# Kernel optimization log

Hardware: AMD Instinct MI355X
Metric: run time of the kernel (lower is better)

The kernel has to match this reference:

```python
import jax, jax.numpy as jnp
import numpy as np

NEG = -1000000000.0


def setup_inputs() -> dict:
    key = jax.random.key(0)
    k1, k2, k3, k4, k5 = jax.random.split(key, 5)
    B, T, D, Q = 8, 2048, 1024, 128
    x = jax.random.normal(k1, (B, T, D), dtype=jnp.float32)
    attn_mask = jax.random.randint(k2, (B, T), 0, 2).astype(jnp.bool_)
    s = 1.0 / np.sqrt(D)
    Wq = jax.random.normal(k3, (Q, D), dtype=jnp.float32) * s
    Wk = jax.random.normal(k4, (Q, D), dtype=jnp.float32) * s
    Wv = jax.random.normal(k5, (Q, D), dtype=jnp.float32) * s
    return {"x": x, "attn_mask": attn_mask, "Wq": Wq, "Wk": Wk, "Wv": Wv}


def reference(x, attn_mask, Wq, Wk, Wv):
    # x: (B,T,D); W*: (Q,D) torch Linear weights (y = x @ W.T)
    q = jnp.einsum('btd,qd->btq', x, Wq)
    k = jnp.einsum('btd,qd->btq', x, Wk)
    v = jnp.einsum('btd,qd->btq', x, Wv)
    logits = jnp.einsum('btq,bsq->bts', q, k)  # (B,T,T), no 1/sqrt(d) scaling (matches source)
    m = attn_mask[:, None, :]  # (B,1,T) broadcasts over query dim, == repeat(1,T,1)
    logits = jnp.where(m, logits, NEG)
    A = jax.nn.softmax(logits, axis=-1)
    A = jnp.where(m, A, 0.0)
    return jnp.einsum('bts,bsq->btq', A, v)
```

## Files before the change

### kernel.cpp

```cpp
#include <hip/hip_runtime.h>
#include <hip/hip_bf16.h>
#include <hip/hip_fp16.h>

typedef _Float16 half8 __attribute__((ext_vector_type(8)));
typedef _Float16 half4v __attribute__((ext_vector_type(4)));
typedef float float4v __attribute__((ext_vector_type(4)));

#define MFMA_F16(a, b, c) __builtin_amdgcn_mfma_f32_16x16x32_f16((a), (b), (c), 0, 0, 0)

#define GLDS16(gp, lp) \
    __builtin_amdgcn_global_load_lds((const __attribute__((address_space(1))) unsigned int*)(gp), \
                                     (__attribute__((address_space(3))) unsigned int*)(lp), 16, 0, 0)

#define BATCH 8
#define SEQ   2048
#define DIM   1024
#define QD    128
#define BT    (BATCH * SEQ)
#define NSPLIT 4
#define KSPAN (SEQ / NSPLIT)

__device__ __forceinline__ float dpp_max16(float x) {
    int v;
    v = __builtin_amdgcn_update_dpp(0, __float_as_int(x), 0xB1, 0xF, 0xF, false);
    x = fmaxf(x, __int_as_float(v));
    v = __builtin_amdgcn_update_dpp(0, __float_as_int(x), 0x4E, 0xF, 0xF, false);
    x = fmaxf(x, __int_as_float(v));
    v = __builtin_amdgcn_update_dpp(0, __float_as_int(x), 0x141, 0xF, 0xF, false);
    x = fmaxf(x, __int_as_float(v));
    v = __builtin_amdgcn_update_dpp(0, __float_as_int(x), 0x140, 0xF, 0xF, false);
    x = fmaxf(x, __int_as_float(v));
    return x;
}

__global__ __launch_bounds__(256) void cvt_w_kernel(const float* __restrict__ Wq,
                                                    const float* __restrict__ Wk,
                                                    const float* __restrict__ Wv,
                                                    _Float16* __restrict__ Wh) {
    const float* src = (blockIdx.y == 0) ? Wq : ((blockIdx.y == 1) ? Wk : Wv);
    int i = blockIdx.x * 256 + threadIdx.x;
    float4 f = ((const float4*)src)[i];
    half4v h = {(_Float16)f.x, (_Float16)f.y, (_Float16)f.z, (_Float16)f.w};
    ((half4v*)(Wh + (size_t)blockIdx.y * QD * DIM))[i] = h;
}

__global__ __launch_bounds__(256, 3) void proj_kernel(
    const float* __restrict__ x,
    const _Float16* __restrict__ Wh,
    _Float16* __restrict__ q_out,
    _Float16* __restrict__ k_out,
    _Float16* __restrict__ vt_out)
{
    __shared__ _Float16 As[64 * 64];
    __shared__ _Float16 Bs[128 * 64];

    const int tid  = threadIdx.x;
    const int lane = tid & 63;
    const int wave = tid >> 6;
    const int quad = lane >> 4;
    const int l15  = lane & 15;
    const int wr   = wave >> 1;
    const int wc   = wave & 1;

    const int which = blockIdx.y;
    const _Float16* W = Wh + (size_t)which * QD * DIM;
    const int row0 = blockIdx.x * 64;

    const int ar  = tid >> 2;
    const int ac4 = tid & 3;
    const float4* xp = (const float4*)(x + (size_t)(row0 + ar) * DIM) + ac4 * 4;
    const int ga = ac4 * 2;
    const int sw = ar & 7;
    _Float16* aw0 = &As[ar * 64 + ((ga     ^ sw) * 8)];
    _Float16* aw1 = &As[ar * 64 + (((ga|1) ^ sw) * 8)];

    float4v acc[2][4];
#pragma unroll
    for (int rf = 0; rf < 2; rf++)
#pragma unroll
        for (int n = 0; n < 4; n++)
            acc[rf][n] = (float4v){0.f, 0.f, 0.f, 0.f};

    for (int kk = 0; kk < DIM; kk += 64) {
        int kb = kk >> 2;
        float4 a0 = xp[kb + 0];
        float4 a1 = xp[kb + 1];
        float4 a2 = xp[kb + 2];
        float4 a3 = xp[kb + 3];
        __syncthreads();
#pragma unroll
        for (int c = 0; c < 4; c++) {
            int ci = wave * 256 + c * 64 + lane;
            int r  = ci >> 3;
            int g  = (ci & 7) ^ (r & 7);
            GLDS16(W + (size_t)r * DIM + kk + g * 8, &Bs[(wave * 256 + c * 64) * 8]);
        }
        half8 h0, h1;
        h0[0] = (_Float16)a0.x; h0[1] = (_Float16)a0.y; h0[2] = (_Float16)a0.z; h0[3] = (_Float16)a0.w;
        h0[4] = (_Float16)a1.x; h0[5] = (_Float16)a1.y; h0[6] = (_Float16)a1.z; h0[7] = (_Float16)a1.w;
        h1[0] = (_Float16)a2.x; h1[1] = (_Float16)a2.y; h1[2] = (_Float16)a2.z; h1[3] = (_Float16)a2.w;
        h1[4] = (_Float16)a3.x; h1[5] = (_Float16)a3.y; h1[6] = (_Float16)a3.z; h1[7] = (_Float16)a3.w;
        *(half8*)aw0 = h0;
        *(half8*)aw1 = h1;
        __syncthreads();

        half8 af[2][2], bf[4][2];
#pragma unroll
        for (int rf = 0; rf < 2; rf++)
#pragma unroll
            for (int kc = 0; kc < 2; kc++) {
                int r = wr * 32 + rf * 16 + l15;
                int g = (kc * 4 + quad) ^ (r & 7);
                af[rf][kc] = *(const half8*)&As[r * 64 + g * 8];
            }
#pragma unroll
        for (int n = 0; n < 4; n++)
#pragma unroll
            for (int kc = 0; kc < 2; kc++) {
                int r = wc * 64 + n * 16 + l15;
                int g = (kc * 4 + quad) ^ (r & 7);
                bf[n][kc] = *(const half8*)&Bs[r * 64 + g * 8];
            }
#pragma unroll
        for (int kc = 0; kc < 2; kc++)
#pragma unroll
            for (int rf = 0; rf < 2; rf++)
#pragma unroll
                for (int n = 0; n < 4; n++)
                    acc[rf][n] = MFMA_F16(af[rf][kc], bf[n][kc], acc[rf][n]);
    }

    if (which == 2) {
#pragma unroll
        for (int rf = 0; rf < 2; rf++) {
            int grow0 = row0 + wr * 32 + rf * 16 + quad * 4;
            int b  = grow0 >> 11;
            int t0 = grow0 & 2047;
#pragma unroll
            for (int n = 0; n < 4; n++) {
                int col = wc * 64 + n * 16 + l15;
                half4v h;
#pragma unroll
                for (int r = 0; r < 4; r++) h[r] = (_Float16)acc[rf][n][r];
                *(half4v*)&vt_out[((size_t)(b * QD + col)) * SEQ + t0] = h;
            }
        }
    } else {
        _Float16* out = (which == 0) ? q_out : k_out;
#pragma unroll
        for (int rf = 0; rf < 2; rf++) {
            int grow0 = row0 + wr * 32 + rf * 16 + quad * 4;
#pragma unroll
            for (int n = 0; n < 4; n++) {
                int col = wc * 64 + n * 16 + l15;
#pragma unroll
                for (int r = 0; r < 4; r++)
                    out[(size_t)(grow0 + r) * QD + col] = (_Float16)acc[rf][n][r];
            }
        }
    }
}

__global__ __launch_bounds__(256, 2) void attn_kernel(
    const _Float16* __restrict__ q,
    const _Float16* __restrict__ k,
    const _Float16* __restrict__ vt,
    const int* __restrict__ mask,
    _Float16* __restrict__ Op,
    float2* __restrict__ ml)
{
    __shared__ _Float16 Ks[64 * 128];
    __shared__ _Float16 Vs[128 * 64];
    __shared__ _Float16 Ps[4 * 32 * 64];
    __shared__ float Msf[64];

    const int tid  = threadIdx.x;
    const int lane = tid & 63;
    const int wave = tid >> 6;
    const int quad = lane >> 4;
    const int l15  = lane & 15;

    const int b  = blockIdx.y;
    const int z  = blockIdx.z;
    const int rowbase = blockIdx.x * 128 + wave * 32;

    half8 qf[2][4];
#pragma unroll
    for (int rf = 0; rf < 2; rf++) {
        const _Float16* qrow = q + ((size_t)(b * SEQ + rowbase + rf * 16 + l15)) * QD + quad * 8;
#pragma unroll
        for (int kc = 0; kc < 4; kc++)
            qf[rf][kc] = *(const half8*)(qrow + kc * 32);
    }

    const half8 onesv = {(_Float16)1, (_Float16)1, (_Float16)1, (_Float16)1,
                         (_Float16)1, (_Float16)1, (_Float16)1, (_Float16)1};

    float4v oacc[2][8];
#pragma unroll
    for (int rf = 0; rf < 2; rf++)
#pragma unroll
        for (int n = 0; n < 8; n++)
            oacc[rf][n] = (float4v){0.f, 0.f, 0.f, 0.f};
    float4v lacc[2] = {(float4v){0.f, 0.f, 0.f, 0.f}, (float4v){0.f, 0.f, 0.f, 0.f}};
    float mrow[2][4];
#pragma unroll
    for (int rf = 0; rf < 2; rf++)
#pragma unroll
        for (int r = 0; r < 4; r++) mrow[rf][r] = -1e30f;

    _Float16* Pw = &Ps[wave * 32 * 64];

    for (int sb = z * KSPAN; sb < z * KSPAN + KSPAN; sb += 64) {
        __syncthreads();
#pragma unroll
        for (int c = 0; c < 4; c++) {
            int ci = wave * 256 + c * 64 + lane;
            int r  = ci >> 4;
            int gs = ci & 15;
            int g  = (gs & 8) | ((gs ^ r) & 7);
            GLDS16(k + ((size_t)(b * SEQ + sb + r)) * QD + g * 8, &Ks[(wave * 256 + c * 64) * 8]);
        }
#pragma unroll
        for (int c = 0; c < 4; c++) {
            int ci = wave * 256 + c * 64 + lane;
            int r  = ci >> 3;
            int g  = ((ci & 7) ^ r) & 7;
            GLDS16(vt + ((size_t)(b * QD + r)) * SEQ + sb + g * 8, &Vs[(wave * 256 + c * 64) * 8]);
        }
        if (tid < 64) Msf[tid] = mask[b * SEQ + sb + tid] ? 0.f : -1e30f;
        __syncthreads();

        float4v sacc[2][4];
#pragma unroll
        for (int rf = 0; rf < 2; rf++)
#pragma unroll
            for (int j = 0; j < 4; j++)
                sacc[rf][j] = (float4v){0.f, 0.f, 0.f, 0.f};
#pragma unroll
        for (int kc = 0; kc < 4; kc++) {
            half8 kf[4];
#pragma unroll
            for (int j = 0; j < 4; j++) {
                int r  = j * 16 + l15;
                int g  = kc * 4 + quad;
                int gs = (g & 8) | ((g ^ r) & 7);
                kf[j] = *(const half8*)&Ks[r * 128 + gs * 8];
            }
#pragma unroll
            for (int rf = 0; rf < 2; rf++)
#pragma unroll
                for (int j = 0; j < 4; j++)
                    sacc[rf][j] = MFMA_F16(qf[rf][kc], kf[j], sacc[rf][j]);
        }

        float alpha[2][4];
#pragma unroll
        for (int rf = 0; rf < 2; rf++) {
            float rmax[4] = {-1e30f, -1e30f, -1e30f, -1e30f};
#pragma unroll
            for (int j = 0; j < 4; j++) {
                float bias = Msf[j * 16 + l15];
#pragma unroll
                for (int r = 0; r < 4; r++) {
                    float s = sacc[rf][j][r] + bias;
                    sacc[rf][j][r] = s;
                    rmax[r] = fmaxf(rmax[r], s);
                }
            }
#pragma unroll
            for (int r = 0; r < 4; r++) {
                float rm = dpp_max16(rmax[r]);
                float mnew = fmaxf(mrow[rf][r], rm);
                alpha[rf][r] = __expf(mrow[rf][r] - mnew);
                mrow[rf][r] = mnew;
            }
        }

#pragma unroll
        for (int rf = 0; rf < 2; rf++)
#pragma unroll
            for (int j = 0; j < 4; j++) {
                int col = j * 16 + l15;
                int gc  = col >> 3;
#pragma unroll
                for (int r = 0; r < 4; r++) {
                    int m  = rf * 16 + quad * 4 + r;
                    int gs = (gc ^ m) & 7;
                    float p = __expf(sacc[rf][j][r] - mrow[rf][r]);
                    Pw[m * 64 + gs * 8 + (col & 7)] = (_Float16)p;
                }
            }

#pragma unroll
        for (int rf = 0; rf < 2; rf++) {
#pragma unroll
            for (int n = 0; n < 8; n++)
#pragma unroll
                for (int r = 0; r < 4; r++)
                    oacc[rf][n][r] *= alpha[rf][r];
#pragma unroll
            for (int r = 0; r < 4; r++) lacc[rf][r] *= alpha[rf][r];
        }

#pragma unroll
        for (int kc = 0; kc < 2; kc++) {
            half8 pf[2];
#pragma unroll
            for (int rf = 0; rf < 2; rf++) {
                int m  = rf * 16 + l15;
                int gs = ((kc * 4 + quad) ^ m) & 7;
                pf[rf] = *(const half8*)&Pw[m * 64 + gs * 8];
            }
#pragma unroll
            for (int n = 0; n < 8; n++) {
                int r  = n * 16 + l15;
                int gs = ((kc * 4 + quad) ^ r) & 7;
                half8 vf = *(const half8*)&Vs[r * 64 + gs * 8];
#pragma unroll
                for (int rf = 0; rf < 2; rf++)
                    oacc[rf][n] = MFMA_F16(pf[rf], vf, oacc[rf][n]);
            }
#pragma unroll
            for (int rf = 0; rf < 2; rf++)
                lacc[rf] = MFMA_F16(pf[rf], onesv, lacc[rf]);
        }
    }

    _Float16* Oz = Op + (size_t)z * BT * QD;
#pragma unroll
    for (int rf = 0; rf < 2; rf++) {
#pragma unroll
        for (int n = 0; n < 8; n++) {
            int col = n * 16 + l15;
#pragma unroll
            for (int r = 0; r < 4; r++) {
                int row = rowbase + rf * 16 + quad * 4 + r;
                Oz[((size_t)(b * SEQ + row)) * QD + col] = (_Float16)oacc[rf][n][r];
            }
        }
        if (l15 == 0) {
#pragma unroll
            for (int r = 0; r < 4; r++) {
                int row = rowbase + rf * 16 + quad * 4 + r;
                ml[(size_t)z * BT + b * SEQ + row] = make_float2(mrow[rf][r], lacc[rf][r]);
            }
        }
    }
}

__global__ __launch_bounds__(256) void merge_kernel(
    const _Float16* __restrict__ Op,
    const float2* __restrict__ ml,
    float* __restrict__ out)
{
    int gid = blockIdx.x * 256 + threadIdx.x;
    int row = gid >> 4;
    int c8  = (gid & 15) * 8;

    float2 a[NSPLIT];
    float m = -3.0e38f;
#pragma unroll
    for (int s = 0; s < NSPLIT; s++) { a[s] = ml[(size_t)s * BT + row]; m = fmaxf(m, a[s].x); }
    float sc[NSPLIT];
    float denom = 0.f;
#pragma unroll
    for (int s = 0; s < NSPLIT; s++) { sc[s] = __expf(a[s].x - m); denom += sc[s] * a[s].y; }
    float inv = (denom > 0.f) ? (1.0f / denom) : 0.f;

    float acc[8] = {0, 0, 0, 0, 0, 0, 0, 0};
#pragma unroll
    for (int s = 0; s < NSPLIT; s++) {
        half8 o = *(const half8*)&Op[(size_t)s * BT * QD + (size_t)row * QD + c8];
#pragma unroll
        for (int e = 0; e < 8; e++) acc[e] += (float)o[e] * sc[s];
    }
    float4 lo = make_float4(acc[0] * inv, acc[1] * inv, acc[2] * inv, acc[3] * inv);
    float4 hi = make_float4(acc[4] * inv, acc[5] * inv, acc[6] * inv, acc[7] * inv);
    *(float4*)&out[(size_t)row * QD + c8] = lo;
    *(float4*)&out[(size_t)row * QD + c8 + 4] = hi;
}

extern "C" void kernel_launch(void* const* d_in, const int* in_sizes, int n_in,
                              void* d_out, int out_size, void* d_ws, size_t ws_size,
                              hipStream_t stream) {
    const float* x    = (const float*)d_in[0];
    const int*   mask = (const int*)d_in[1];
    const float* Wq   = (const float*)d_in[2];
    const float* Wk   = (const float*)d_in[3];
    const float* Wv   = (const float*)d_in[4];
    float* out = (float*)d_out;

    char* p = (char*)d_ws;
    _Float16* Wh  = (_Float16*)p; p += (size_t)3 * QD * DIM * 2;
    _Float16* qb  = (_Float16*)p; p += (size_t)BT * QD * 2;
    _Float16* kb  = (_Float16*)p; p += (size_t)BT * QD * 2;
    _Float16* vtb = (_Float16*)p; p += (size_t)BT * QD * 2;
    _Float16* Op  = (_Float16*)p; p += (size_t)NSPLIT * BT * QD * 2;
    float2*   ml  = (float2*)p;

    cvt_w_kernel<<<dim3(QD * DIM / 4 / 256, 3), 256, 0, stream>>>(Wq, Wk, Wv, Wh);
    proj_kernel<<<dim3(BT / 64, 3), 256, 0, stream>>>(x, Wh, qb, kb, vtb);
    attn_kernel<<<dim3(SEQ / 128, BATCH, NSPLIT), 256, 0, stream>>>(qb, kb, vtb, mask, Op, ml);
    merge_kernel<<<dim3(BT * 16 / 256), 256, 0, stream>>>(Op, ml, out);
}
```

Measured before the change: 163.9 us.

## Fuse Q/K/V projections into one block per tile with double-buffered LDS

Each block now computes all three projections for its 64-row tile, so x is loaded from global memory and converted to half once instead of three times. Shared-memory tiles for x and the three weight slices are double-buffered, so the next k-step's loads overlap the current MFMAs. This trades occupancy for reuse: the kernel now uses much more LDS and holds three accumulator sets, and launch bounds drop to one block per CU.

```diff
diff --git a/kernel.cpp b/kernel.cpp
--- a/kernel.cpp
+++ b/kernel.cpp
@@ -44,15 +44,15 @@
     ((half4v*)(Wh + (size_t)blockIdx.y * QD * DIM))[i] = h;
 }
 
-__global__ __launch_bounds__(256, 3) void proj_kernel(
+__global__ __launch_bounds__(256, 1) void proj_kernel(
     const float* __restrict__ x,
     const _Float16* __restrict__ Wh,
     _Float16* __restrict__ q_out,
     _Float16* __restrict__ k_out,
     _Float16* __restrict__ vt_out)
 {
-    __shared__ _Float16 As[64 * 64];
-    __shared__ _Float16 Bs[128 * 64];
+    __shared__ _Float16 As[2][64 * 64];
+    __shared__ _Float16 Bs[2][3][128 * 64];
 
     const int tid  = threadIdx.x;
     const int lane = tid & 63;
@@ -62,100 +62,146 @@
     const int wr   = wave >> 1;
     const int wc   = wave & 1;
 
-    const int which = blockIdx.y;
-    const _Float16* W = Wh + (size_t)which * QD * DIM;
     const int row0 = blockIdx.x * 64;
 
     const int ar  = tid >> 2;
     const int ac4 = tid & 3;
-    const float4* xp = (const float4*)(x + (size_t)(row0 + ar) * DIM) + ac4 * 4;
-    const int ga = ac4 * 2;
-    const int sw = ar & 7;
-    _Float16* aw0 = &As[ar * 64 + ((ga     ^ sw) * 8)];
-    _Float16* aw1 = &As[ar * 64 + (((ga|1) ^ sw) * 8)];
-
-    float4v acc[2][4];
-#pragma unroll
-    for (int rf = 0; rf < 2; rf++)
-#pragma unroll
-        for (int n = 0; n < 4; n++)
-            acc[rf][n] = (float4v){0.f, 0.f, 0.f, 0.f};
-
-    for (int kk = 0; kk < DIM; kk += 64) {
-        int kb = kk >> 2;
-        float4 a0 = xp[kb + 0];
-        float4 a1 = xp[kb + 1];
-        float4 a2 = xp[kb + 2];
-        float4 a3 = xp[kb + 3];
-        __syncthreads();
-#pragma unroll
-        for (int c = 0; c < 4; c++) {
-            int ci = wave * 256 + c * 64 + lane;
-            int r  = ci >> 3;
-            int g  = (ci & 7) ^ (r & 7);
-            GLDS16(W + (size_t)r * DIM + kk + g * 8, &Bs[(wave * 256 + c * 64) * 8]);
+    const float* xp = x + (size_t)(row0 + ar) * DIM + ac4 * 16;
+    const int ga  = ac4 * 2;
+    const int sw  = ar & 7;
+    const int aw0 = ar * 64 + ((ga       ^ sw) * 8);
+    const int aw1 = ar * 64 + (((ga | 1) ^ sw) * 8);
+
+    float4v acc[3][2][4];
+#pragma unroll
+    for (int m = 0; m < 3; m++)
+#pragma unroll
+        for (int rf = 0; rf < 2; rf++)
+#pragma unroll
+            for (int n = 0; n < 4; n++)
+                acc[m][rf][n] = (float4v){0.f, 0.f, 0.f, 0.f};
+
+    {
+        float4 a0 = *(const float4*)(xp + 0);
+        float4 a1 = *(const float4*)(xp + 4);
+        float4 a2 = *(const float4*)(xp + 8);
+        float4 a3 = *(const float4*)(xp + 12);
+#pragma unroll
+        for (int m = 0; m < 3; m++) {
+            const _Float16* W = Wh + (size_t)m * QD * DIM;
+#pragma unroll
+            for (int c = 0; c < 4; c++) {
+                int ci = wave * 256 + c * 64 + lane;
+                int r  = ci >> 3;
+                int g  = (ci & 7) ^ (r & 7);
+                GLDS16(W + (size_t)r * DIM + g * 8, &Bs[0][m][(wave * 256 + c * 64) * 8]);
+            }
         }
         half8 h0, h1;
         h0[0] = (_Float16)a0.x; h0[1] = (_Float16)a0.y; h0[2] = (_Float16)a0.z; h0[3] = (_Float16)a0.w;
         h0[4] = (_Float16)a1.x; h0[5] = (_Float16)a1.y; h0[6] = (_Float16)a1.z; h0[7] = (_Float16)a1.w;
         h1[0] = (_Float16)a2.x; h1[1] = (_Float16)a2.y; h1[2] = (_Float16)a2.z; h1[3] = (_Float16)a2.w;
         h1[4] = (_Float16)a3.x; h1[5] = (_Float16)a3.y; h1[6] = (_Float16)a3.z; h1[7] = (_Float16)a3.w;
-        *(half8*)aw0 = h0;
-        *(half8*)aw1 = h1;
-        __syncthreads();
-
-        half8 af[2][2], bf[4][2];
+        *(half8*)&As[0][aw0] = h0;
+        *(half8*)&As[0][aw1] = h1;
+    }
+    __syncthreads();
+
+    for (int t = 0; t < 16; t++) {
+        const int cur = t & 1;
+        const int nxt = cur ^ 1;
+
+        float4 b0, b1, b2, b3;
+        if (t < 15) {
+            const float* xq = xp + (t + 1) * 64;
+            b0 = *(const float4*)(xq + 0);
+            b1 = *(const float4*)(xq + 4);
+            b2 = *(const float4*)(xq + 8);
+            b3 = *(const float4*)(xq + 12);
+            const int kkn = (t + 1) * 64;
+#pragma unroll
+            for (int m = 0; m < 3; m++) {
+                const _Float16* W = Wh + (size_t)m * QD * DIM + kkn;
+#pragma unroll
+                for (int c = 0; c < 4; c++) {
+                    int ci = wave * 256 + c * 64 + lane;
+                    int r  = ci >> 3;
+                    int g  = (ci & 7) ^ (r & 7);
+                    GLDS16(W + (size_t)r * DIM + g * 8, &Bs[nxt][m][(wave * 256 + c * 64) * 8]);
+                }
+            }
+        }
+
+        half8 af[2][2];
 #pragma unroll
         for (int rf = 0; rf < 2; rf++)
 #pragma unroll
             for (int kc = 0; kc < 2; kc++) {
                 int r = wr * 32 + rf * 16 + l15;
                 int g = (kc * 4 + quad) ^ (r & 7);
-                af[rf][kc] = *(const half8*)&As[r * 64 + g * 8];
-            }
-#pragma unroll
-        for (int n = 0; n < 4; n++)
-#pragma unroll
-            for (int kc = 0; kc < 2; kc++) {
-                int r = wc * 64 + n * 16 + l15;
-                int g = (kc * 4 + quad) ^ (r & 7);
-                bf[n][kc] = *(const half8*)&Bs[r * 64 + g * 8];
-            }
-#pragma unroll
-        for (int kc = 0; kc < 2; kc++)
-#pragma unroll
-            for (int rf = 0; rf < 2; rf++)
-#pragma unroll
-                for (int n = 0; n < 4; n++)
-                    acc[rf][n] = MFMA_F16(af[rf][kc], bf[n][kc], acc[rf][n]);
-    }
-
-    if (which == 2) {
-#pragma unroll
-        for (int rf = 0; rf < 2; rf++) {
-            int grow0 = row0 + wr * 32 + rf * 16 + quad * 4;
-            int b  = grow0 >> 11;
-            int t0 = grow0 & 2047;
-#pragma unroll
-            for (int n = 0; n < 4; n++) {
-                int col = wc * 64 + n * 16 + l15;
-                half4v h;
-#pragma unroll
-                for (int r = 0; r < 4; r++) h[r] = (_Float16)acc[rf][n][r];
-                *(half4v*)&vt_out[((size_t)(b * QD + col)) * SEQ + t0] = h;
-            }
-        }
-    } else {
-        _Float16* out = (which == 0) ? q_out : k_out;
-#pragma unroll
-        for (int rf = 0; rf < 2; rf++) {
-            int grow0 = row0 + wr * 32 + rf * 16 + quad * 4;
-#pragma unroll
-            for (int n = 0; n < 4; n++) {
-                int col = wc * 64 + n * 16 + l15;
-#pragma unroll
-                for (int r = 0; r < 4; r++)
-                    out[(size_t)(grow0 + r) * QD + col] = (_Float16)acc[rf][n][r];
+                af[rf][kc] = *(const half8*)&As[cur][r * 64 + g * 8];
+            }
+#pragma unroll
+        for (int m = 0; m < 3; m++) {
+            half8 bf[4][2];
+#pragma unroll
+            for (int n = 0; n < 4; n++)
+#pragma unroll
+                for (int kc = 0; kc < 2; kc++) {
+                    int r = wc * 64 + n * 16 + l15;
+                    int g = (kc * 4 + quad) ^ (r & 7);
+                    bf[n][kc] = *(const half8*)&Bs[cur][m][r * 64 + g * 8];
+                }
+#pragma unroll
+            for (int kc = 0; kc < 2; kc++)
+#pragma unroll
+                for (int rf = 0; rf < 2; rf++)
+#pragma unroll
+                    for (int n = 0; n < 4; n++)
+                        acc[m][rf][n] = MFMA_F16(af[rf][kc], bf[n][kc], acc[m][rf][n]);
+        }
+
+        if (t < 15) {
+            half8 h0, h1;
+            h0[0] = (_Float16)b0.x; h0[1] = (_Float16)b0.y; h0[2] = (_Float16)b0.z; h0[3] = (_Float16)b0.w;
+            h0[4] = (_Float16)b1.x; h0[5] = (_Float16)b1.y; h0[6] = (_Float16)b1.z; h0[7] = (_Float16)b1.w;
+            h1[0] = (_Float16)b2.x; h1[1] = (_Float16)b2.y; h1[2] = (_Float16)b2.z; h1[3] = (_Float16)b2.w;
+            h1[4] = (_Float16)b3.x; h1[5] = (_Float16)b3.y; h1[6] = (_Float16)b3.z; h1[7] = (_Float16)b3.w;
+            *(half8*)&As[nxt][aw0] = h0;
+            *(half8*)&As[nxt][aw1] = h1;
+        }
+        __syncthreads();
+    }
+
+#pragma unroll
+    for (int m = 0; m < 3; m++) {
+        if (m == 2) {
+#pragma unroll
+            for (int rf = 0; rf < 2; rf++) {
+                int grow0 = row0 + wr * 32 + rf * 16 + quad * 4;
+                int b  = grow0 >> 11;
+                int t0 = grow0 & 2047;
+#pragma unroll
+                for (int n = 0; n < 4; n++) {
+                    int col = wc * 64 + n * 16 + l15;
+                    half4v h;
+#pragma unroll
+                    for (int r = 0; r < 4; r++) h[r] = (_Float16)acc[m][rf][n][r];
+                    *(half4v*)&vt_out[((size_t)(b * QD + col)) * SEQ + t0] = h;
+                }
+            }
+        } else {
+            _Float16* out = (m == 0) ? q_out : k_out;
+#pragma unroll
+            for (int rf = 0; rf < 2; rf++) {
+                int grow0 = row0 + wr * 32 + rf * 16 + quad * 4;
+#pragma unroll
+                for (int n = 0; n < 4; n++) {
+                    int col = wc * 64 + n * 16 + l15;
+#pragma unroll
+                    for (int r = 0; r < 4; r++)
+                        out[(size_t)(grow0 + r) * QD + col] = (_Float16)acc[m][rf][n][r];
+                }
             }
         }
     }
@@ -400,7 +446,7 @@
     float2*   ml  = (float2*)p;
 
     cvt_w_kernel<<<dim3(QD * DIM / 4 / 256, 3), 256, 0, stream>>>(Wq, Wk, Wv, Wh);
-    proj_kernel<<<dim3(BT / 64, 3), 256, 0, stream>>>(x, Wh, qb, kb, vtb);
+    proj_kernel<<<dim3(BT / 64), 256, 0, stream>>>(x, Wh, qb, kb, vtb);
     attn_kernel<<<dim3(SEQ / 128, BATCH, NSPLIT), 256, 0, stream>>>(qb, kb, vtb, mask, Op, ml);
     merge_kernel<<<dim3(BT * 16 / 256), 256, 0, stream>>>(Op, ml, out);
 }
```

Result: no change. 164.8 us (+0.5%).
